# Kernel tuning notes

Hardware: AMD Instinct MI355X
Metric: run time of the kernel (lower is better)

## Reference

```python
import jax, jax.numpy as jnp
import numpy as np

LUT_VALS = np.array([-1.0, -0.5, -0.333333, -0.2, -0.142857, -0.090909, -0.076923,
                     0.0, 0.076923, 0.090909, 0.142857, 0.2, 0.333333, 0.5, 1.0],
                    dtype=np.float32)

B, S, IN, OUT = 4, 2048, 2048, 8192


def setup_inputs() -> dict:
    key = jax.random.key(0)
    kx, ki = jax.random.split(key)
    x = jax.random.normal(kx, (B, S, IN), dtype=jnp.float32)
    # uint8 LUT indices into the 15-entry primal grid (stored int32 for jax indexing)
    grid_indices = jax.random.randint(ki, (OUT, IN), 0, 15, dtype=jnp.int32)
    scale = jnp.float32(1.0)
    lut = jnp.asarray(LUT_VALS)
    return {"x": x, "grid_indices": grid_indices, "scale": scale, "lut": lut}


def reference(x, grid_indices, scale, lut):
    # Dequantize: gather LUT values by index, then scalar scale (GhostQuantFunction.forward)
    weights = lut[grid_indices] * scale          # [OUT, IN] fp32
    # F.linear(x, weights): y = x @ W^T
    return jnp.einsum('bsi,oi->bso', x, weights)
```

## Files before the change

kernel.cpp:

```cpp
#include <hip/hip_runtime.h>
#include <cstdint>

typedef short bf16x8 __attribute__((ext_vector_type(8)));
typedef unsigned short u16x8 __attribute__((ext_vector_type(8)));
typedef float f32x4 __attribute__((ext_vector_type(4)));
typedef __attribute__((address_space(3))) uint32_t lds_u32;
typedef const __attribute__((address_space(1))) uint32_t gbl_u32;

__device__ __forceinline__ unsigned short f2bf(float f) {
  union { float f; uint32_t u; } c; c.f = f;
  uint32_t u = c.u;
  return (unsigned short)((u + 0x7fffu + ((u >> 16) & 1u)) >> 16);
}

__global__ void cvt_x_kernel(const float* __restrict__ x,
                             unsigned short* __restrict__ y, long n) {
  long t = (long)blockIdx.x * blockDim.x + threadIdx.x;
  long base = t * 8;
  if (base >= n) return;
  const float4* p = (const float4*)(x + base);
  float4 f0 = p[0], f1 = p[1];
  u16x8 v;
  v[0] = f2bf(f0.x); v[1] = f2bf(f0.y); v[2] = f2bf(f0.z); v[3] = f2bf(f0.w);
  v[4] = f2bf(f1.x); v[5] = f2bf(f1.y); v[6] = f2bf(f1.z); v[7] = f2bf(f1.w);
  *(u16x8*)(y + base) = v;
}

__global__ void dequant_kernel(const int* __restrict__ idx,
                               const float* __restrict__ lut,
                               const float* __restrict__ scale,
                               unsigned short* __restrict__ w, long n) {
  __shared__ unsigned short slut[16];
  if (threadIdx.x < 15) slut[threadIdx.x] = f2bf(lut[threadIdx.x] * scale[0]);
  __syncthreads();
  long t = (long)blockIdx.x * blockDim.x + threadIdx.x;
  long base = t * 8;
  if (base >= n) return;
  const int4* p = (const int4*)(idx + base);
  int4 i0 = p[0], i1 = p[1];
  u16x8 v;
  v[0] = slut[i0.x]; v[1] = slut[i0.y]; v[2] = slut[i0.z]; v[3] = slut[i0.w];
  v[4] = slut[i1.x]; v[5] = slut[i1.y]; v[6] = slut[i1.z]; v[7] = slut[i1.w];
  *(u16x8*)(w + base) = v;
}

__global__ __launch_bounds__(256) void gemm_bt(
    const unsigned short* __restrict__ A,
    const unsigned short* __restrict__ B,
    float* __restrict__ C, int M, int N, int K) {
  __shared__ unsigned short lA[128 * 32];
  __shared__ unsigned short lB[128 * 32];

  const int t = threadIdx.x;
  const int l = t & 63;
  const int w = t >> 6;
  const int wm = w >> 1, wn = w & 1;
  const int bm = blockIdx.y, bn = blockIdx.x;

  f32x4 acc[4][4] = {};

  const unsigned short* gA = A + (size_t)(bm * 128 + (t >> 2)) * K + (t & 3) * 8;
  const unsigned short* gB = B + (size_t)(bn * 128 + (t >> 2)) * K + (t & 3) * 8;
  lds_u32* sA = (lds_u32*)(&lA[0]) + t * 4;
  lds_u32* sB = (lds_u32*)(&lB[0]) + t * 4;

  const int ar = wm * 64 + (l & 15);
  const int br = wn * 64 + (l & 15);
  const int ak = (l >> 4) * 8;

  for (int kt = 0; kt < K; kt += 32) {
    __syncthreads();
    __builtin_amdgcn_global_load_lds((gbl_u32*)(gA + kt),          sA,        16, 0, 0);
    __builtin_amdgcn_global_load_lds((gbl_u32*)(gA + 64 * K + kt), sA + 1024, 16, 0, 0);
    __builtin_amdgcn_global_load_lds((gbl_u32*)(gB + kt),          sB,        16, 0, 0);
    __builtin_amdgcn_global_load_lds((gbl_u32*)(gB + 64 * K + kt), sB + 1024, 16, 0, 0);
    __syncthreads();

    bf16x8 af[4], bfr[4];
#pragma unroll
    for (int i = 0; i < 4; ++i)
      af[i] = *(const bf16x8*)&lA[(ar + i * 16) * 32 + ak];
#pragma unroll
    for (int j = 0; j < 4; ++j)
      bfr[j] = *(const bf16x8*)&lB[(br + j * 16) * 32 + ak];
#pragma unroll
    for (int i = 0; i < 4; ++i)
#pragma unroll
      for (int j = 0; j < 4; ++j)
        acc[i][j] = __builtin_amdgcn_mfma_f32_16x16x32_bf16(af[i], bfr[j], acc[i][j], 0, 0, 0);
  }

  float* Cp = C + (size_t)(bm * 128 + wm * 64 + (l >> 4) * 4) * N
              + bn * 128 + wn * 64 + (l & 15);
#pragma unroll
  for (int i = 0; i < 4; ++i)
#pragma unroll
    for (int j = 0; j < 4; ++j)
#pragma unroll
      for (int r = 0; r < 4; ++r)
        Cp[(size_t)(i * 16 + r) * N + j * 16] = acc[i][j][r];
}

extern "C" void kernel_launch(void* const* d_in, const int* in_sizes, int n_in,
                              void* d_out, int out_size, void* d_ws, size_t ws_size,
                              hipStream_t stream) {
  const float* x     = (const float*)d_in[0];
  const int*   gi    = (const int*)d_in[1];
  const float* scale = (const float*)d_in[2];
  const float* lut   = (const float*)d_in[3];
  float* out = (float*)d_out;

  const int M = 8192, N = 8192, K = 2048;
  unsigned short* xb = (unsigned short*)d_ws;
  unsigned short* wb = xb + (size_t)M * K;

  long nx = (long)M * K;
  long nw = (long)N * K;
  cvt_x_kernel<<<dim3((unsigned)(nx / (256 * 8))), dim3(256), 0, stream>>>(x, xb, nx);
  dequant_kernel<<<dim3((unsigned)(nw / (256 * 8))), dim3(256), 0, stream>>>(gi, lut, scale, wb, nw);

  dim3 grid(N / 128, M / 128);
  gemm_bt<<<grid, dim3(256), 0, stream>>>(xb, wb, out, M, N, K);
}
```

Baseline: 666.4 us.

## Rewrite GEMM as 256x256 double-buffered pipelined kernel with swizzled LDS

Replaces the 128x128 single-buffered GEMM with a 256x256-tile, 512-thread kernel. It double-buffers the LDS, splitting each 64-wide k-tile into four quarter stages that are prefetched with global_load_lds while MFMAs run, using raw barriers and waitcnt. It also XOR-swizzles the LDS layout to avoid bank conflicts, remaps block IDs for L2 locality, and raises MFMA priority with setprio. The aim is to hide global load latency and raise arithmetic intensity, at the cost of heavy register and LDS use and fragile hand-tuned synchronization.

New measurement: 602.7 us. -9.6%, faster.

```diff
diff --git a/kernel.cpp b/kernel.cpp
--- a/kernel.cpp
+++ b/kernel.cpp
@@ -44,56 +44,143 @@
   *(u16x8*)(w + base) = v;
 }
 
-__global__ __launch_bounds__(256) void gemm_bt(
+
+__device__ __forceinline__ void bar() {
+  asm volatile("" ::: "memory");
+  __builtin_amdgcn_s_barrier();
+  asm volatile("" ::: "memory");
+}
+
+#define STAGE(D, R, G, KOFF)                                                  \
+  do {                                                                        \
+    lds_u32* dst_ = (lds_u32*)(&lds[0]) + (D) * 16384 + (R) * 4096 + t * 4;   \
+    const unsigned short* s_ = (G) + (KOFF);                                  \
+    __builtin_amdgcn_global_load_lds((gbl_u32*)(s_), dst_, 16, 0, 0);         \
+    __builtin_amdgcn_global_load_lds((gbl_u32*)(s_ + (size_t)128 * 2048),     \
+                                     dst_ + 2048, 16, 0, 0);                  \
+  } while (0)
+
+template <int D>
+__device__ __forceinline__ void ktile(int T, unsigned short* lds,
+                                      f32x4 (&acc)[8][4],
+                                      const unsigned short* gA,
+                                      const unsigned short* gB, int t,
+                                      int aoff, int boff) {
+  constexpr int NT = 32;
+  const int c1 = (T + 1 < NT) ? (T + 1) : (NT - 1);
+  const int c2 = (T + 2 < NT) ? (T + 2) : (NT - 1);
+  const int k1 = c1 * 64, k2 = c2 * 64;
+
+  const unsigned short* lA0 = &lds[D * 32768 + aoff];
+  const unsigned short* lA1 = &lds[D * 32768 + 8192 + aoff];
+  const unsigned short* lB0 = &lds[D * 32768 + 16384 + boff];
+  const unsigned short* lB1 = &lds[D * 32768 + 24576 + boff];
+
+  bf16x8 afr[8], b0, b1;
+
+#pragma unroll
+  for (int i = 0; i < 8; ++i) afr[i] = *(const bf16x8*)(lA0 + i * 512);
+  b0 = *(const bf16x8*)(lB0);
+  b1 = *(const bf16x8*)(lB0 + 512);
+  STAGE(D ^ 1, 3, gB, k1 + 32);
+  bar();
+  __builtin_amdgcn_s_setprio(1);
+#pragma unroll
+  for (int i = 0; i < 8; ++i) {
+    acc[i][0] = __builtin_amdgcn_mfma_f32_16x16x32_bf16(afr[i], b0, acc[i][0], 0, 0, 0);
+    acc[i][1] = __builtin_amdgcn_mfma_f32_16x16x32_bf16(afr[i], b1, acc[i][1], 0, 0, 0);
+  }
+  __builtin_amdgcn_s_setprio(0);
+  bar();
+
+  b0 = *(const bf16x8*)(lB0 + 1024);
+  b1 = *(const bf16x8*)(lB0 + 1536);
+  STAGE(D ^ 1, 1, gA, k1 + 32);
+  bar();
+  __builtin_amdgcn_s_setprio(1);
+#pragma unroll
+  for (int i = 0; i < 8; ++i) {
+    acc[i][2] = __builtin_amdgcn_mfma_f32_16x16x32_bf16(afr[i], b0, acc[i][2], 0, 0, 0);
+    acc[i][3] = __builtin_amdgcn_mfma_f32_16x16x32_bf16(afr[i], b1, acc[i][3], 0, 0, 0);
+  }
+  __builtin_amdgcn_s_setprio(0);
+  bar();
+
+#pragma unroll
+  for (int i = 0; i < 8; ++i) afr[i] = *(const bf16x8*)(lA1 + i * 512);
+  b0 = *(const bf16x8*)(lB1);
+  b1 = *(const bf16x8*)(lB1 + 512);
+  STAGE(D, 0, gA, k2);
+  bar();
+  __builtin_amdgcn_s_setprio(1);
+#pragma unroll
+  for (int i = 0; i < 8; ++i) {
+    acc[i][0] = __builtin_amdgcn_mfma_f32_16x16x32_bf16(afr[i], b0, acc[i][0], 0, 0, 0);
+    acc[i][1] = __builtin_amdgcn_mfma_f32_16x16x32_bf16(afr[i], b1, acc[i][1], 0, 0, 0);
+  }
+  __builtin_amdgcn_s_setprio(0);
+  bar();
+
+  b0 = *(const bf16x8*)(lB1 + 1024);
+  b1 = *(const bf16x8*)(lB1 + 1536);
+  STAGE(D, 2, gB, k2);
+  bar();
+  __builtin_amdgcn_s_setprio(1);
+#pragma unroll
+  for (int i = 0; i < 8; ++i) {
+    acc[i][2] = __builtin_amdgcn_mfma_f32_16x16x32_bf16(afr[i], b0, acc[i][2], 0, 0, 0);
+    acc[i][3] = __builtin_amdgcn_mfma_f32_16x16x32_bf16(afr[i], b1, acc[i][3], 0, 0, 0);
+  }
+  __builtin_amdgcn_s_setprio(0);
+  asm volatile("s_waitcnt vmcnt(4)" ::: "memory");
+  bar();
+}
+
+__global__ __launch_bounds__(512, 2) void gemm_bt_256(
     const unsigned short* __restrict__ A,
     const unsigned short* __restrict__ B,
-    float* __restrict__ C, int M, int N, int K) {
-  __shared__ unsigned short lA[128 * 32];
-  __shared__ unsigned short lB[128 * 32];
+    float* __restrict__ C) {
+  constexpr int K = 2048, N = 8192, NT = 32;
+  __shared__ unsigned short lds[65536];
 
   const int t = threadIdx.x;
   const int l = t & 63;
   const int w = t >> 6;
-  const int wm = w >> 1, wn = w & 1;
-  const int bm = blockIdx.y, bn = blockIdx.x;
-
-  f32x4 acc[4][4] = {};
-
-  const unsigned short* gA = A + (size_t)(bm * 128 + (t >> 2)) * K + (t & 3) * 8;
-  const unsigned short* gB = B + (size_t)(bn * 128 + (t >> 2)) * K + (t & 3) * 8;
-  lds_u32* sA = (lds_u32*)(&lA[0]) + t * 4;
-  lds_u32* sB = (lds_u32*)(&lB[0]) + t * 4;
-
-  const int ar = wm * 64 + (l & 15);
-  const int br = wn * 64 + (l & 15);
-  const int ak = (l >> 4) * 8;
-
-  for (int kt = 0; kt < K; kt += 32) {
-    __syncthreads();
-    __builtin_amdgcn_global_load_lds((gbl_u32*)(gA + kt),          sA,        16, 0, 0);
-    __builtin_amdgcn_global_load_lds((gbl_u32*)(gA + 64 * K + kt), sA + 1024, 16, 0, 0);
-    __builtin_amdgcn_global_load_lds((gbl_u32*)(gB + kt),          sB,        16, 0, 0);
-    __builtin_amdgcn_global_load_lds((gbl_u32*)(gB + 64 * K + kt), sB + 1024, 16, 0, 0);
-    __syncthreads();
-
-    bf16x8 af[4], bfr[4];
-#pragma unroll
-    for (int i = 0; i < 4; ++i)
-      af[i] = *(const bf16x8*)&lA[(ar + i * 16) * 32 + ak];
-#pragma unroll
-    for (int j = 0; j < 4; ++j)
-      bfr[j] = *(const bf16x8*)&lB[(br + j * 16) * 32 + ak];
-#pragma unroll
-    for (int i = 0; i < 4; ++i)
-#pragma unroll
-      for (int j = 0; j < 4; ++j)
-        acc[i][j] = __builtin_amdgcn_mfma_f32_16x16x32_bf16(af[i], bfr[j], acc[i][j], 0, 0, 0);
-  }
-
-  float* Cp = C + (size_t)(bm * 128 + wm * 64 + (l >> 4) * 4) * N
-              + bn * 128 + wn * 64 + (l & 15);
-#pragma unroll
-  for (int i = 0; i < 4; ++i)
+  const int wm = w >> 2, wn = w & 3;
+
+  const int bid = blockIdx.x;
+  const int swz = (bid & 7) * 128 + (bid >> 3);
+  const int bm = swz >> 5, bn = swz & 31;
+
+  f32x4 acc[8][4] = {};
+
+  const int lchunk = (t & 3) ^ ((t >> 5) & 1);
+  const unsigned short* gA = A + (size_t)(bm * 256 + (t >> 2)) * K + lchunk * 8;
+  const unsigned short* gB = B + (size_t)(bn * 256 + (t >> 2)) * K + lchunk * 8;
+
+  const int sc8 = ((l >> 4) ^ ((l >> 3) & 1)) * 8;
+  const int aoff = (wm * 128 + (l & 15)) * 32 + sc8;
+  const int boff = (wn * 64 + (l & 15)) * 32 + sc8;
+
+  STAGE(0, 0, gA, 0);
+  STAGE(0, 2, gB, 0);
+  STAGE(0, 3, gB, 32);
+  STAGE(0, 1, gA, 32);
+  STAGE(1, 0, gA, 64);
+  STAGE(1, 2, gB, 64);
+  asm volatile("s_waitcnt vmcnt(4)" ::: "memory");
+  bar();
+
+  for (int T = 0; T < NT; T += 2) {
+    ktile<0>(T, lds, acc, gA, gB, t, aoff, boff);
+    ktile<1>(T + 1, lds, acc, gA, gB, t, aoff, boff);
+  }
+  asm volatile("s_waitcnt vmcnt(0)" ::: "memory");
+
+  float* Cp = C + (size_t)(bm * 256 + wm * 128 + ((l >> 4) << 2)) * N
+              + bn * 256 + wn * 64 + (l & 15);
+#pragma unroll
+  for (int i = 0; i < 8; ++i)
 #pragma unroll
     for (int j = 0; j < 4; ++j)
 #pragma unroll
@@ -119,6 +206,5 @@
   cvt_x_kernel<<<dim3((unsigned)(nx / (256 * 8))), dim3(256), 0, stream>>>(x, xb, nx);
   dequant_kernel<<<dim3((unsigned)(nw / (256 * 8))), dim3(256), 0, stream>>>(gi, lut, scale, wb, nw);
 
-  dim3 grid(N / 128, M / 128);
-  gemm_bt<<<grid, dim3(256), 0, stream>>>(xb, wb, out, M, N, K);
-}
+  gemm_bt_256<<<dim3((M / 256) * (N / 256)), dim3(512), 0, stream>>>(xb, wb, out);
+}
```
